# Kernel optimization log

Hardware: AMD Instinct MI355X
Metric: run time of the kernel (lower is better)

## Reference

```python
import jax, jax.numpy as jnp
import numpy as np
import math

B, S, V, E, D, H, L = 1024, 30, 100000, 300, 512, 8, 4
DK = D // H

def setup_inputs() -> dict:
    key = jax.random.key(0)
    ks = jax.random.split(key, 12)
    sc = 0.02
    return {
        "x": jax.random.randint(ks[0], (B, S), 0, V, dtype=jnp.int32),
        "mask": jax.random.randint(ks[1], (B, 1, 1, S), 0, 2, dtype=jnp.int32),
        "emb": jax.random.normal(ks[2], (V, E), dtype=jnp.float32) * sc,
        "W_in": jax.random.normal(ks[3], (D, E), dtype=jnp.float32) * sc,
        "b_in": jnp.zeros((D,), jnp.float32),
        "Wq": jax.random.normal(ks[4], (L, DK, DK), dtype=jnp.float32) * 0.05,
        "Wk": jax.random.normal(ks[5], (L, DK, DK), dtype=jnp.float32) * 0.05,
        "Wv": jax.random.normal(ks[6], (L, DK, DK), dtype=jnp.float32) * 0.05,
        "Wo": jax.random.normal(ks[7], (L, D, D), dtype=jnp.float32) * sc,
        "Wfc": jax.random.normal(ks[8], (L, D, D), dtype=jnp.float32) * sc,
        "bfc": jnp.zeros((L, D), jnp.float32),
        "g1": jnp.ones((L, D), jnp.float32),
        "beta1": jnp.zeros((L, D), jnp.float32),
        "g2": jnp.ones((L, D), jnp.float32),
        "beta2": jnp.zeros((L, D), jnp.float32),
    }

def _layernorm(x, g, b, eps=1e-5):
    mu = jnp.mean(x, axis=-1, keepdims=True)
    var = jnp.mean(jnp.square(x - mu), axis=-1, keepdims=True)
    return (x - mu) * jax.lax.rsqrt(var + eps) * g + b

def _pos_encoding():
    pos = jnp.arange(S, dtype=jnp.float32)[:, None]
    div = jnp.exp(jnp.arange(0, D, 2, dtype=jnp.float32) * (-math.log(10000.0) / D))
    ang = pos * div  # [S, D/2]
    pe = jnp.zeros((S, D), jnp.float32)
    pe = pe.at[:, 0::2].set(jnp.sin(ang)).at[:, 1::2].set(jnp.cos(ang))
    return pe

def _block(h, mask, Wq, Wk, Wv, Wo, Wfc, bfc, g1, b1, g2, b2):
    xh = h.reshape(B, S, H, DK)
    # per-head shared d_k x d_k projections (nn.Linear: y = x @ W.T)
    q = jnp.einsum('bshk,dk->bhsd', xh, Wq)
    k = jnp.einsum('bshk,dk->bhsd', xh, Wk)
    v = jnp.einsum('bshk,dk->bhsd', xh, Wv)
    scores = jnp.einsum('bhqd,bhkd->bhqk', q, k) / math.sqrt(DK)
    scores = jnp.where(mask == 0, jnp.float32(-1e9), scores)
    p = jax.nn.softmax(scores, axis=-1)
    o = jnp.einsum('bhqk,bhkd->bqhd', p, v).reshape(B, S, D)
    o = o @ Wo.T  # output projection, no bias
    n1 = _layernorm(o + h, g1, b1)
    f = n1 @ Wfc.T + bfc
    return _layernorm(f + n1, g2, b2)

def reference(x, mask, emb, W_in, b_in, Wq, Wk, Wv, Wo, Wfc, bfc, g1, beta1, g2, beta2):
    h = emb[x]                               # [B,S,E] embedding gather
    h = jnp.einsum('bse,de->bsd', h, W_in) + b_in
    h = h * math.sqrt(D) + _pos_encoding()[None]  # positional encoding (dropout=eval no-op)
    for i in range(L):
        h = _block(h, mask, Wq[i], Wk[i], Wv[i], Wo[i], Wfc[i], bfc[i],
                   g1[i], beta1[i], g2[i], beta2[i])
    return h
```

## Files before the change

kernel.cpp:

```cpp
#include <hip/hip_runtime.h>
#include <hip/hip_bf16.h>
#include <math.h>

using bf16 = __hip_bfloat16;
typedef __attribute__((ext_vector_type(8))) short short8;
typedef __attribute__((ext_vector_type(4))) float f32x4;

constexpr int nB = 1024, nS = 30, nE = 300, nD = 512, nH = 8, nL = 4, nDK = 64;
constexpr int nTOK = nB * nS;
constexpr float kSqrtD = 22.627416997969522f;
constexpr float kPEc   = -0.03597789207803244f;

__device__ inline unsigned short bfbits(float f) {
  bf16 h = __float2bfloat16(f);
  return *(unsigned short*)&h;
}
__device__ inline void gload16(const void* g, void* lds) {
  __builtin_amdgcn_global_load_lds(
      (const __attribute__((address_space(1))) unsigned int*)g,
      (__attribute__((address_space(3))) unsigned int*)lds, 16, 0, 0);
}

__global__ __launch_bounds__(256) void cvt_kernel(const float* __restrict__ s,
                                                  bf16* __restrict__ d, int n4) {
  int i = blockIdx.x * 256 + threadIdx.x;
  if (i < n4) {
    float4 v = ((const float4*)s)[i];
    ushort4 u;
    u.x = bfbits(v.x); u.y = bfbits(v.y); u.z = bfbits(v.z); u.w = bfbits(v.w);
    ((ushort4*)d)[i] = u;
  }
}

__global__ __launch_bounds__(256) void cvt_pad_win(const float* __restrict__ s,
                                                   bf16* __restrict__ d) {
  int row = blockIdx.x;
  for (int e = threadIdx.x; e < 320; e += 256)
    d[row * 320 + e] = __float2bfloat16((e < nE) ? s[row * nE + e] : 0.f);
}

__global__ __launch_bounds__(256) void pe_kernel(float* __restrict__ pe) {
  int s = blockIdx.x;
  for (int dd = threadIdx.x; dd < nD; dd += 256) {
    float ang = (float)s * expf((float)(dd >> 1) * kPEc);
    pe[s * nD + dd] = (dd & 1) ? cosf(ang) : sinf(ang);
  }
}

__global__ __launch_bounds__(256) void gather_kernel(const int* __restrict__ x,
                                                     const float* __restrict__ emb,
                                                     bf16* __restrict__ a) {
  int g = blockIdx.x * 256 + threadIdx.x;
  int t = g / 40, ch = g - 40 * t;
  float4 v0 = make_float4(0.f, 0.f, 0.f, 0.f), v1 = v0;
  const float* src = emb + (size_t)x[t] * nE + ch * 8;
  if (ch < 37) { v0 = *(const float4*)src; v1 = *(const float4*)(src + 4); }
  else if (ch == 37) { v0 = *(const float4*)src; }
  ushort4 u0, u1;
  u0.x = bfbits(v0.x); u0.y = bfbits(v0.y); u0.z = bfbits(v0.z); u0.w = bfbits(v0.w);
  u1.x = bfbits(v1.x); u1.y = bfbits(v1.y); u1.z = bfbits(v1.z); u1.w = bfbits(v1.w);
  bf16* dst = a + (size_t)t * 320 + ch * 8;
  *(ushort4*)dst = u0;
  *(ushort4*)(dst + 4) = u1;
}

template <int KA, int EPI>
__global__ __launch_bounds__(256, 2) void gemm_fused(
    const bf16* __restrict__ A, const bf16* __restrict__ W,
    const float* __restrict__ bias, const float* __restrict__ resid,
    const float* __restrict__ pe, const float* __restrict__ g,
    const float* __restrict__ beta, float* __restrict__ outf,
    bf16* __restrict__ outb) {
  __shared__ __align__(16) char smem[39424];
  bf16* As = (bf16*)smem;
  bf16* Ws = (bf16*)smem + 2048;
  float* tb = (float*)smem;
  float* stats = (float*)(smem + 36864);
  float* stats2 = (float*)(smem + 38912);

  const int tid = threadIdx.x, lane = tid & 63, w = tid >> 6;
  const int q = lane >> 4, c = lane & 15;
  const int m0 = blockIdx.x * 64;

  f32x4 acc[4][8];
#pragma unroll
  for (int i = 0; i < 4; ++i)
#pragma unroll
    for (int j = 0; j < 8; ++j) acc[i][j] = (f32x4){0.f, 0.f, 0.f, 0.f};

  const bf16* Ag = A + (size_t)(m0 + lane) * KA + w * 8;
  const bf16* Wg = W + (size_t)lane * KA + w * 8;
  bf16* AsDst = As + (w * 64) * 8;
  bf16* WsDst = Ws + (w * 512) * 8;

  for (int ks = 0; ks < KA / 32; ++ks) {
    __syncthreads();
    gload16(Ag + ks * 32, AsDst);
#pragma unroll
    for (int j = 0; j < 8; ++j)
      gload16(Wg + (size_t)(j * 64) * KA + ks * 32, WsDst + j * 64 * 8);
    __syncthreads();
    short8 af[4], bfr[8];
#pragma unroll
    for (int mt = 0; mt < 4; ++mt)
      af[mt] = *(const short8*)(As + (q * 64 + mt * 16 + c) * 8);
#pragma unroll
    for (int nt = 0; nt < 8; ++nt)
      bfr[nt] = *(const short8*)(Ws + (q * 512 + w * 128 + nt * 16 + c) * 8);
#pragma unroll
    for (int mt = 0; mt < 4; ++mt)
#pragma unroll
      for (int nt = 0; nt < 8; ++nt)
        acc[mt][nt] = __builtin_amdgcn_mfma_f32_16x16x32_bf16(af[mt], bfr[nt], acc[mt][nt], 0, 0, 0);
  }

  float bias4[8];
#pragma unroll
  for (int nt = 0; nt < 8; ++nt)
    bias4[nt] = bias ? bias[w * 128 + nt * 16 + c] : 0.f;

  if (EPI == 0) {
#pragma unroll
    for (int mt = 0; mt < 4; ++mt)
#pragma unroll
      for (int r = 0; r < 4; ++r) {
        int m = m0 + mt * 16 + q * 4 + r;
        int s = m % nS;
        const float* pes = pe + (size_t)s * nD + w * 128 + c;
#pragma unroll
        for (int nt = 0; nt < 8; ++nt)
          acc[mt][nt][r] = (acc[mt][nt][r] + bias4[nt]) * kSqrtD + pes[nt * 16];
      }
    __syncthreads();
  } else {
    float rs[4][4], rq[4][4];
#pragma unroll
    for (int mt = 0; mt < 4; ++mt)
#pragma unroll
      for (int r = 0; r < 4; ++r) {
        int m = m0 + mt * 16 + q * 4 + r;
        const float* rp = resid + (size_t)m * nD + w * 128 + c;
        float s1 = 0.f, s2 = 0.f;
#pragma unroll
        for (int nt = 0; nt < 8; ++nt) {
          float t = acc[mt][nt][r] + bias4[nt] + rp[nt * 16];
          acc[mt][nt][r] = t;
          s1 += t; s2 += t * t;
        }
        rs[mt][r] = s1; rq[mt][r] = s2;
      }
#pragma unroll
    for (int mt = 0; mt < 4; ++mt)
#pragma unroll
      for (int r = 0; r < 4; ++r)
#pragma unroll
        for (int off = 1; off < 16; off <<= 1) {
          rs[mt][r] += __shfl_xor(rs[mt][r], off);
          rq[mt][r] += __shfl_xor(rq[mt][r], off);
        }
#pragma unroll
    for (int mt = 0; mt < 4; ++mt)
#pragma unroll
      for (int r = 0; r < 4; ++r)
        if (c == mt * 4 + r) {
          int row = mt * 16 + q * 4 + r;
          stats[row * 8 + w * 2] = rs[mt][r];
          stats[row * 8 + w * 2 + 1] = rq[mt][r];
        }
    __syncthreads();
    if (tid < 64) {
      float su = 0.f, sq = 0.f;
#pragma unroll
      for (int ww = 0; ww < 4; ++ww) {
        su += stats[tid * 8 + ww * 2];
        sq += stats[tid * 8 + ww * 2 + 1];
      }
      float mu = su * (1.f / nD);
      float var = sq * (1.f / nD) - mu * mu;
      stats2[tid * 2] = mu;
      stats2[tid * 2 + 1] = rsqrtf(var + 1e-5f);
    }
    __syncthreads();
  }

  float* tbw = tb + w * 2048;
  const int l32 = lane & 31, hi = lane >> 5;
  const int colw = w * 128 + l32 * 4;
  float4 g4 = make_float4(0, 0, 0, 0), be4 = g4;
  if (EPI == 1) {
    g4 = *(const float4*)&g[colw];
    be4 = *(const float4*)&beta[colw];
  }
#pragma unroll
  for (int mt = 0; mt < 4; ++mt) {
#pragma unroll
    for (int nt = 0; nt < 8; ++nt)
#pragma unroll
      for (int r = 0; r < 4; ++r)
        tbw[(q * 4 + r) * 128 + nt * 16 + c] = acc[mt][nt][r];
#pragma unroll
    for (int i = 0; i < 8; ++i) {
      float4 v = *(const float4*)&tbw[(i * 64 + lane) * 4];
      int rl = mt * 16 + i * 2 + hi;
      int m = m0 + rl;
      float4 y;
      if (EPI == 1) {
        float mu = stats2[rl * 2], inv = stats2[rl * 2 + 1];
        y.x = (v.x - mu) * inv * g4.x + be4.x;
        y.y = (v.y - mu) * inv * g4.y + be4.y;
        y.z = (v.z - mu) * inv * g4.z + be4.z;
        y.w = (v.w - mu) * inv * g4.w + be4.w;
      } else {
        y = v;
      }
      *(float4*)(outf + (size_t)m * nD + colw) = y;
      ushort4 ub;
      ub.x = bfbits(y.x); ub.y = bfbits(y.y); ub.z = bfbits(y.z); ub.w = bfbits(y.w);
      *(ushort4*)(outb + (size_t)m * nD + colw) = ub;
    }
  }
}

__global__ __launch_bounds__(256) void attn_kernel(
    const bf16* __restrict__ wqb, const bf16* __restrict__ wkb,
    const bf16* __restrict__ wvb, const int* __restrict__ mask,
    bf16* __restrict__ hb) {
  const int tid = threadIdx.x, lane = tid & 63, w = tid >> 6;
  const int q = lane >> 4, c = lane & 15;
  const int b = blockIdx.x >> 3, hd = blockIdx.x & 7;

  __shared__ __align__(16) bf16 xs[8][32][8];
  __shared__ __align__(16) bf16 wq[8][64][8];
  __shared__ __align__(16) bf16 wk[8][64][8];
  __shared__ __align__(16) bf16 wv[8][64][8];
  __shared__ __align__(16) bf16 qb[8][32][8];
  __shared__ __align__(16) bf16 kb[8][32][8];
  __shared__ __align__(16) bf16 vt[4][64][8];
  __shared__ __align__(16) bf16 pb[4][32][8];
  __shared__ float ps[32][33];
  __shared__ int msk[32];

  {
    int row = tid & 31, k8 = tid >> 5;
    uint4 z = make_uint4(0, 0, 0, 0);
    if (row < nS)
      z = *(const uint4*)(hb + (size_t)(b * nS + row) * nD + hd * nDK + k8 * 8);
    *(uint4*)&xs[k8][row][0] = z;
  }
#pragma unroll
  for (int i = 0; i < 2; ++i) {
    int s = tid + i * 256;
    int row = s & 63, k8 = s >> 6;
    *(uint4*)&wq[k8][row][0] = *(const uint4*)(wqb + row * 64 + k8 * 8);
    *(uint4*)&wk[k8][row][0] = *(const uint4*)(wkb + row * 64 + k8 * 8);
    *(uint4*)&wv[k8][row][0] = *(const uint4*)(wvb + row * 64 + k8 * 8);
  }
  if (tid < nS) msk[tid] = mask[b * nS + tid];
  __syncthreads();

  f32x4 aq[2], ak[2], av[2];
#pragma unroll
  for (int mt = 0; mt < 2; ++mt) {
    aq[mt] = (f32x4){0.f, 0.f, 0.f, 0.f};
    ak[mt] = aq[mt]; av[mt] = aq[mt];
  }
#pragma unroll
  for (int kc = 0; kc < 2; ++kc) {
    short8 xa0 = *(const short8*)&xs[kc * 4 + q][c][0];
    short8 xa1 = *(const short8*)&xs[kc * 4 + q][16 + c][0];
    short8 wqf = *(const short8*)&wq[kc * 4 + q][w * 16 + c][0];
    short8 wkf = *(const short8*)&wk[kc * 4 + q][w * 16 + c][0];
    short8 wvf = *(const short8*)&wv[kc * 4 + q][w * 16 + c][0];
    aq[0] = __builtin_amdgcn_mfma_f32_16x16x32_bf16(xa0, wqf, aq[0], 0, 0, 0);
    aq[1] = __builtin_amdgcn_mfma_f32_16x16x32_bf16(xa1, wqf, aq[1], 0, 0, 0);
    ak[0] = __builtin_amdgcn_mfma_f32_16x16x32_bf16(xa0, wkf, ak[0], 0, 0, 0);
    ak[1] = __builtin_amdgcn_mfma_f32_16x16x32_bf16(xa1, wkf, ak[1], 0, 0, 0);
    av[0] = __builtin_amdgcn_mfma_f32_16x16x32_bf16(xa0, wvf, av[0], 0, 0, 0);
    av[1] = __builtin_amdgcn_mfma_f32_16x16x32_bf16(xa1, wvf, av[1], 0, 0, 0);
  }
  const int dk = w * 16 + c;
#pragma unroll
  for (int mt = 0; mt < 2; ++mt)
#pragma unroll
    for (int r = 0; r < 4; ++r) {
      int i = mt * 16 + q * 4 + r;
      qb[dk >> 3][i][dk & 7] = __float2bfloat16(aq[mt][r]);
      kb[dk >> 3][i][dk & 7] = __float2bfloat16(ak[mt][r]);
      vt[i >> 3][dk][i & 7] = __float2bfloat16(av[mt][r]);
    }
  __syncthreads();

  {
    f32x4 sc = (f32x4){0.f, 0.f, 0.f, 0.f};
    const int is0 = (w >> 1) * 16, js0 = (w & 1) * 16;
#pragma unroll
    for (int kc = 0; kc < 2; ++kc) {
      short8 a = *(const short8*)&qb[kc * 4 + q][is0 + c][0];
      short8 bb = *(const short8*)&kb[kc * 4 + q][js0 + c][0];
      sc = __builtin_amdgcn_mfma_f32_16x16x32_bf16(a, bb, sc, 0, 0, 0);
    }
    int j = js0 + c;
    bool live = (j < nS) && (msk[j] != 0);
#pragma unroll
    for (int r = 0; r < 4; ++r) {
      int i = is0 + q * 4 + r;
      ps[i][j] = live ? sc[r] * 0.125f : -1e9f;
    }
  }
  __syncthreads();

  if (tid < nS * 8) {
    int r = tid >> 3, cc = tid & 7;
    float m = -1e30f;
    for (int j = cc; j < nS; j += 8) m = fmaxf(m, ps[r][j]);
#pragma unroll
    for (int o = 1; o < 8; o <<= 1) m = fmaxf(m, __shfl_xor(m, o));
    float sum = 0.f;
    for (int j = cc; j < nS; j += 8) sum += __expf(ps[r][j] - m);
#pragma unroll
    for (int o = 1; o < 8; o <<= 1) sum += __shfl_xor(sum, o);
    float inv = 1.f / sum;
    for (int j = cc; j < nS; j += 8)
      pb[j >> 3][r][j & 7] = __float2bfloat16(__expf(ps[r][j] - m) * inv);
    if (cc >= 6) pb[3][r][cc] = __float2bfloat16(0.f);
  }
  __syncthreads();

  {
    f32x4 o0 = (f32x4){0.f, 0.f, 0.f, 0.f}, o1 = o0;
    short8 pa0 = *(const short8*)&pb[q][c][0];
    short8 pa1 = *(const short8*)&pb[q][16 + c][0];
    short8 vb = *(const short8*)&vt[q][w * 16 + c][0];
    o0 = __builtin_amdgcn_mfma_f32_16x16x32_bf16(pa0, vb, o0, 0, 0, 0);
    o1 = __builtin_amdgcn_mfma_f32_16x16x32_bf16(pa1, vb, o1, 0, 0, 0);
#pragma unroll
    for (int r = 0; r < 4; ++r) {
      int i0 = q * 4 + r;
      hb[(size_t)(b * nS + i0) * nD + hd * nDK + dk] = __float2bfloat16(o0[r]);
      int i1 = 16 + q * 4 + r;
      if (i1 < nS)
        hb[(size_t)(b * nS + i1) * nD + hd * nDK + dk] = __float2bfloat16(o1[r]);
    }
  }
}

extern "C" void kernel_launch(void* const* d_in, const int* in_sizes, int n_in,
                              void* d_out, int out_size, void* d_ws, size_t ws_size,
                              hipStream_t stream) {
  const int*   x    = (const int*)d_in[0];
  const int*   mask = (const int*)d_in[1];
  const float* emb  = (const float*)d_in[2];
  const float* W_in = (const float*)d_in[3];
  const float* b_in = (const float*)d_in[4];
  const float* Wq   = (const float*)d_in[5];
  const float* Wk   = (const float*)d_in[6];
  const float* Wv   = (const float*)d_in[7];
  const float* Wo   = (const float*)d_in[8];
  const float* Wfc  = (const float*)d_in[9];
  const float* bfc  = (const float*)d_in[10];
  const float* g1   = (const float*)d_in[11];
  const float* be1  = (const float*)d_in[12];
  const float* g2   = (const float*)d_in[13];
  const float* be2  = (const float*)d_in[14];
  float* h = (float*)d_out;

  char* ws = (char*)d_ws;
  bf16* wo_b  = (bf16*)ws;
  bf16* wfc_b = (bf16*)(ws + 2097152);
  bf16* wq_b  = (bf16*)(ws + 4194304);
  bf16* wk_b  = (bf16*)(ws + 4227072);
  bf16* wv_b  = (bf16*)(ws + 4259840);
  bf16* win_b = (bf16*)(ws + 4292608);
  float* pe   = (float*)(ws + 4620288);
  bf16* a_emb = (bf16*)(ws + 4681728);
  bf16* hb    = (bf16*)(ws + 24342528);

  cvt_kernel<<<1024, 256, 0, stream>>>(Wo, wo_b, 262144);
  cvt_kernel<<<1024, 256, 0, stream>>>(Wfc, wfc_b, 262144);
  cvt_kernel<<<16, 256, 0, stream>>>(Wq, wq_b, 4096);
  cvt_kernel<<<16, 256, 0, stream>>>(Wk, wk_b, 4096);
  cvt_kernel<<<16, 256, 0, stream>>>(Wv, wv_b, 4096);
  cvt_pad_win<<<512, 256, 0, stream>>>(W_in, win_b);
  pe_kernel<<<30, 256, 0, stream>>>(pe);
  gather_kernel<<<4800, 256, 0, stream>>>(x, emb, a_emb);

  gemm_fused<320, 0><<<480, 256, 0, stream>>>(a_emb, win_b, b_in, nullptr, pe,
                                              nullptr, nullptr, h, hb);
  for (int l = 0; l < nL; ++l) {
    attn_kernel<<<nB * nH, 256, 0, stream>>>(wq_b + l * 4096, wk_b + l * 4096,
                                             wv_b + l * 4096, mask, hb);
    gemm_fused<512, 1><<<480, 256, 0, stream>>>(hb, wo_b + (size_t)l * 262144,
                                                nullptr, h, nullptr, g1 + l * nD,
                                                be1 + l * nD, h, hb);
    gemm_fused<512, 1><<<480, 256, 0, stream>>>(hb, wfc_b + (size_t)l * 262144,
                                                bfc + l * nD, h, nullptr, g2 + l * nD,
                                                be2 + l * nD, h, hb);
  }
  (void)in_sizes; (void)n_in; (void)out_size; (void)ws_size;
}
```

Measured before the change: 695.7 us.

## Double-buffer GEMM K-loop LDS staging with async global loads

Converts the single-buffered K-loop of the fused GEMM into a two-stage ping-pong pipeline. The next K-slice is issued with global_load_lds into the alternate LDS buffer before the MFMA work on the current one, and a partial vmcnt wait covers only the older loads. This is meant to hide global-memory latency behind compute. It roughly doubles shared memory per block (about 76KB), which may reduce blocks per CU against the launch bound of 2, and it relies on hand-tuned waitcnt counts.

```diff
diff --git a/kernel.cpp b/kernel.cpp
--- a/kernel.cpp
+++ b/kernel.cpp
@@ -71,16 +71,15 @@
     const float* __restrict__ pe, const float* __restrict__ g,
     const float* __restrict__ beta, float* __restrict__ outf,
     bf16* __restrict__ outb) {
-  __shared__ __align__(16) char smem[39424];
-  bf16* As = (bf16*)smem;
-  bf16* Ws = (bf16*)smem + 2048;
+  __shared__ __align__(16) char smem[76288];
   float* tb = (float*)smem;
-  float* stats = (float*)(smem + 36864);
-  float* stats2 = (float*)(smem + 38912);
+  float* stats = (float*)(smem + 73728);
+  float* stats2 = (float*)(smem + 75776);
 
   const int tid = threadIdx.x, lane = tid & 63, w = tid >> 6;
   const int q = lane >> 4, c = lane & 15;
   const int m0 = blockIdx.x * 64;
+  constexpr int NK = KA / 32;
 
   f32x4 acc[4][8];
 #pragma unroll
@@ -90,16 +89,29 @@
 
   const bf16* Ag = A + (size_t)(m0 + lane) * KA + w * 8;
   const bf16* Wg = W + (size_t)lane * KA + w * 8;
-  bf16* AsDst = As + (w * 64) * 8;
-  bf16* WsDst = Ws + (w * 512) * 8;
-
-  for (int ks = 0; ks < KA / 32; ++ks) {
-    __syncthreads();
-    gload16(Ag + ks * 32, AsDst);
+
+  auto stage = [&](int ks, int buf) {
+    bf16* As = (bf16*)(smem + buf * 36864);
+    bf16* Ws = As + 2048;
+    gload16(Ag + ks * 32, As + (w * 64) * 8);
 #pragma unroll
     for (int j = 0; j < 8; ++j)
-      gload16(Wg + (size_t)(j * 64) * KA + ks * 32, WsDst + j * 64 * 8);
-    __syncthreads();
+      gload16(Wg + (size_t)(j * 64) * KA + ks * 32, Ws + ((size_t)(w * 512 + j * 64)) * 8);
+  };
+
+  stage(0, 0);
+  for (int ks = 0; ks < NK; ++ks) {
+    const int cur = ks & 1;
+    if (ks + 1 < NK) {
+      stage(ks + 1, cur ^ 1);
+      asm volatile("s_waitcnt vmcnt(9)" ::: "memory");
+    } else {
+      asm volatile("s_waitcnt vmcnt(0)" ::: "memory");
+    }
+    __builtin_amdgcn_s_barrier();
+    asm volatile("" ::: "memory");
+    const bf16* As = (const bf16*)(smem + cur * 36864);
+    const bf16* Ws = As + 2048;
     short8 af[4], bfr[8];
 #pragma unroll
     for (int mt = 0; mt < 4; ++mt)
@@ -112,6 +124,9 @@
 #pragma unroll
       for (int nt = 0; nt < 8; ++nt)
         acc[mt][nt] = __builtin_amdgcn_mfma_f32_16x16x32_bf16(af[mt], bfr[nt], acc[mt][nt], 0, 0, 0);
+    asm volatile("" ::: "memory");
+    __builtin_amdgcn_s_barrier();
+    asm volatile("" ::: "memory");
   }
 
   float bias4[8];
```

Result: slower. 740.2 us (+6.4%).

## Keep residual stream in bf16 only and fuse weight-prep kernels into one launch

Applied to the files above, without the earlier changes.

Replaces the fp32 residual stream with bf16 ping-pong buffers: GEMM epilogues now read the residual as bf16 and write either bf16 (intermediate layers) or fp32 (final layer only). Attention reads and writes separate buffers instead of working in place. The seven weight-conversion and positional-encoding launches are merged into a single kernel. This cuts global memory traffic per layer and launch overhead, at the cost of extra rounding because the residual is carried in bf16.

```diff
diff --git a/kernel.cpp b/kernel.cpp
--- a/kernel.cpp
+++ b/kernel.cpp
@@ -15,35 +15,46 @@
   bf16 h = __float2bfloat16(f);
   return *(unsigned short*)&h;
 }
+__device__ inline float b2f(short s) {
+  return __uint_as_float(((unsigned)(unsigned short)s) << 16);
+}
 __device__ inline void gload16(const void* g, void* lds) {
   __builtin_amdgcn_global_load_lds(
       (const __attribute__((address_space(1))) unsigned int*)g,
       (__attribute__((address_space(3))) unsigned int*)lds, 16, 0, 0);
 }
 
-__global__ __launch_bounds__(256) void cvt_kernel(const float* __restrict__ s,
-                                                  bf16* __restrict__ d, int n4) {
+__global__ __launch_bounds__(256) void cvt_all(
+    const float* __restrict__ Wo, const float* __restrict__ Wfc,
+    const float* __restrict__ Wq, const float* __restrict__ Wk,
+    const float* __restrict__ Wv, const float* __restrict__ Win,
+    bf16* __restrict__ wo, bf16* __restrict__ wfc, bf16* __restrict__ wq,
+    bf16* __restrict__ wk, bf16* __restrict__ wv, bf16* __restrict__ win,
+    float* __restrict__ pe) {
   int i = blockIdx.x * 256 + threadIdx.x;
-  if (i < n4) {
-    float4 v = ((const float4*)s)[i];
-    ushort4 u;
-    u.x = bfbits(v.x); u.y = bfbits(v.y); u.z = bfbits(v.z); u.w = bfbits(v.w);
-    ((ushort4*)d)[i] = u;
-  }
-}
-
-__global__ __launch_bounds__(256) void cvt_pad_win(const float* __restrict__ s,
-                                                   bf16* __restrict__ d) {
-  int row = blockIdx.x;
-  for (int e = threadIdx.x; e < 320; e += 256)
-    d[row * 320 + e] = __float2bfloat16((e < nE) ? s[row * nE + e] : 0.f);
-}
-
-__global__ __launch_bounds__(256) void pe_kernel(float* __restrict__ pe) {
-  int s = blockIdx.x;
-  for (int dd = threadIdx.x; dd < nD; dd += 256) {
-    float ang = (float)s * expf((float)(dd >> 1) * kPEc);
-    pe[s * nD + dd] = (dd & 1) ? cosf(ang) : sinf(ang);
+  if (i < 1048576) {
+    wo[i] = __float2bfloat16(Wo[i]);
+    wfc[i] = __float2bfloat16(Wfc[i]);
+    return;
+  }
+  i -= 1048576;
+  if (i < 16384) {
+    wq[i] = __float2bfloat16(Wq[i]);
+    wk[i] = __float2bfloat16(Wk[i]);
+    wv[i] = __float2bfloat16(Wv[i]);
+    return;
+  }
+  i -= 16384;
+  if (i < 163840) {
+    int r = i / 320, e = i - r * 320;
+    win[i] = __float2bfloat16(e < nE ? Win[r * nE + e] : 0.f);
+    return;
+  }
+  i -= 163840;
+  if (i < 15360) {
+    int s = i >> 9, d = i & 511;
+    float ang = (float)s * expf((float)(d >> 1) * kPEc);
+    pe[i] = (d & 1) ? cosf(ang) : sinf(ang);
   }
 }
 
@@ -64,10 +75,10 @@
   *(ushort4*)(dst + 4) = u1;
 }
 
-template <int KA, int EPI>
+template <int KA, int EPI, int FIN>
 __global__ __launch_bounds__(256, 2) void gemm_fused(
     const bf16* __restrict__ A, const bf16* __restrict__ W,
-    const float* __restrict__ bias, const float* __restrict__ resid,
+    const float* __restrict__ bias, const bf16* __restrict__ resid,
     const float* __restrict__ pe, const float* __restrict__ g,
     const float* __restrict__ beta, float* __restrict__ outf,
     bf16* __restrict__ outb) {
@@ -139,11 +150,11 @@
 #pragma unroll
       for (int r = 0; r < 4; ++r) {
         int m = m0 + mt * 16 + q * 4 + r;
-        const float* rp = resid + (size_t)m * nD + w * 128 + c;
+        const short* rp = (const short*)(resid + (size_t)m * nD + w * 128 + c);
         float s1 = 0.f, s2 = 0.f;
 #pragma unroll
         for (int nt = 0; nt < 8; ++nt) {
-          float t = acc[mt][nt][r] + bias4[nt] + rp[nt * 16];
+          float t = acc[mt][nt][r] + bias4[nt] + b2f(rp[nt * 16]);
           acc[mt][nt][r] = t;
           s1 += t; s2 += t * t;
         }
@@ -213,10 +224,13 @@
       } else {
         y = v;
       }
-      *(float4*)(outf + (size_t)m * nD + colw) = y;
-      ushort4 ub;
-      ub.x = bfbits(y.x); ub.y = bfbits(y.y); ub.z = bfbits(y.z); ub.w = bfbits(y.w);
-      *(ushort4*)(outb + (size_t)m * nD + colw) = ub;
+      if (FIN) {
+        *(float4*)(outf + (size_t)m * nD + colw) = y;
+      } else {
+        ushort4 ub;
+        ub.x = bfbits(y.x); ub.y = bfbits(y.y); ub.z = bfbits(y.z); ub.w = bfbits(y.w);
+        *(ushort4*)(outb + (size_t)m * nD + colw) = ub;
+      }
     }
   }
 }
@@ -224,7 +238,7 @@
 __global__ __launch_bounds__(256) void attn_kernel(
     const bf16* __restrict__ wqb, const bf16* __restrict__ wkb,
     const bf16* __restrict__ wvb, const int* __restrict__ mask,
-    bf16* __restrict__ hb) {
+    const bf16* __restrict__ hin, bf16* __restrict__ aout) {
   const int tid = threadIdx.x, lane = tid & 63, w = tid >> 6;
   const int q = lane >> 4, c = lane & 15;
   const int b = blockIdx.x >> 3, hd = blockIdx.x & 7;
@@ -244,7 +258,7 @@
     int row = tid & 31, k8 = tid >> 5;
     uint4 z = make_uint4(0, 0, 0, 0);
     if (row < nS)
-      z = *(const uint4*)(hb + (size_t)(b * nS + row) * nD + hd * nDK + k8 * 8);
+      z = *(const uint4*)(hin + (size_t)(b * nS + row) * nD + hd * nDK + k8 * 8);
     *(uint4*)&xs[k8][row][0] = z;
   }
 #pragma unroll
@@ -336,10 +350,10 @@
 #pragma unroll
     for (int r = 0; r < 4; ++r) {
       int i0 = q * 4 + r;
-      hb[(size_t)(b * nS + i0) * nD + hd * nDK + dk] = __float2bfloat16(o0[r]);
+      aout[(size_t)(b * nS + i0) * nD + hd * nDK + dk] = __float2bfloat16(o0[r]);
       int i1 = 16 + q * 4 + r;
       if (i1 < nS)
-        hb[(size_t)(b * nS + i1) * nD + hd * nDK + dk] = __float2bfloat16(o1[r]);
+        aout[(size_t)(b * nS + i1) * nD + hd * nDK + dk] = __float2bfloat16(o1[r]);
     }
   }
 }
@@ -362,7 +376,6 @@
   const float* be1  = (const float*)d_in[12];
   const float* g2   = (const float*)d_in[13];
   const float* be2  = (const float*)d_in[14];
-  float* h = (float*)d_out;
 
   char* ws = (char*)d_ws;
   bf16* wo_b  = (bf16*)ws;
@@ -373,28 +386,32 @@
   bf16* win_b = (bf16*)(ws + 4292608);
   float* pe   = (float*)(ws + 4620288);
   bf16* a_emb = (bf16*)(ws + 4681728);
-  bf16* hb    = (bf16*)(ws + 24342528);
-
-  cvt_kernel<<<1024, 256, 0, stream>>>(Wo, wo_b, 262144);
-  cvt_kernel<<<1024, 256, 0, stream>>>(Wfc, wfc_b, 262144);
-  cvt_kernel<<<16, 256, 0, stream>>>(Wq, wq_b, 4096);
-  cvt_kernel<<<16, 256, 0, stream>>>(Wk, wk_b, 4096);
-  cvt_kernel<<<16, 256, 0, stream>>>(Wv, wv_b, 4096);
-  cvt_pad_win<<<512, 256, 0, stream>>>(W_in, win_b);
-  pe_kernel<<<30, 256, 0, stream>>>(pe);
+  bf16* bufH  = (bf16*)(ws + 24342528);
+  bf16* bufO  = (bf16*)(ws + 55799808);
+  bf16* bufN  = (bf16*)(ws + 87257088);
+
+  cvt_all<<<4860, 256, 0, stream>>>(Wo, Wfc, Wq, Wk, Wv, W_in, wo_b, wfc_b,
+                                    wq_b, wk_b, wv_b, win_b, pe);
   gather_kernel<<<4800, 256, 0, stream>>>(x, emb, a_emb);
 
-  gemm_fused<320, 0><<<480, 256, 0, stream>>>(a_emb, win_b, b_in, nullptr, pe,
-                                              nullptr, nullptr, h, hb);
+  gemm_fused<320, 0, 0><<<480, 256, 0, stream>>>(
+      a_emb, win_b, b_in, nullptr, pe, nullptr, nullptr, nullptr, bufH);
+
   for (int l = 0; l < nL; ++l) {
-    attn_kernel<<<nB * nH, 256, 0, stream>>>(wq_b + l * 4096, wk_b + l * 4096,
-                                             wv_b + l * 4096, mask, hb);
-    gemm_fused<512, 1><<<480, 256, 0, stream>>>(hb, wo_b + (size_t)l * 262144,
-                                                nullptr, h, nullptr, g1 + l * nD,
-                                                be1 + l * nD, h, hb);
-    gemm_fused<512, 1><<<480, 256, 0, stream>>>(hb, wfc_b + (size_t)l * 262144,
-                                                bfc + l * nD, h, nullptr, g2 + l * nD,
-                                                be2 + l * nD, h, hb);
+    attn_kernel<<<nB * nH, 256, 0, stream>>>(
+        wq_b + l * 4096, wk_b + l * 4096, wv_b + l * 4096, mask, bufH, bufO);
+    gemm_fused<512, 1, 0><<<480, 256, 0, stream>>>(
+        bufO, wo_b + (size_t)l * 262144, nullptr, bufH, nullptr, g1 + l * nD,
+        be1 + l * nD, nullptr, bufN);
+    if (l < nL - 1) {
+      gemm_fused<512, 1, 0><<<480, 256, 0, stream>>>(
+          bufN, wfc_b + (size_t)l * 262144, bfc + l * nD, bufN, nullptr,
+          g2 + l * nD, be2 + l * nD, nullptr, bufH);
+    } else {
+      gemm_fused<512, 1, 1><<<480, 256, 0, stream>>>(
+          bufN, wfc_b + (size_t)l * 262144, bfc + l * nD, bufN, nullptr,
+          g2 + l * nD, be2 + l * nD, (float*)d_out, nullptr);
+    }
   }
   (void)in_sizes; (void)n_in; (void)out_size; (void)ws_size;
 }
```

New measurement: 637.1 us (median of 2 runs). -8.4%, faster.
